# Kernel tuning notes

Measured on AMD Instinct MI355X. Metric: run time of the kernel, lower is better.

## Reference

```python
import jax, jax.numpy as jnp
import numpy as np

B, G, C, K = 16, 2048, 128, 16


def setup_inputs() -> dict:
    key = jax.random.key(0)
    k1, k2, k3, k4 = jax.random.split(key, 4)
    xyz = jax.random.normal(k1, (B, G, 3), dtype=jnp.float32)
    feat = jax.random.normal(k2, (B, G, C), dtype=jnp.float32)
    # MLP params: Linear(C->C) -> GELU -> Linear(C->C)
    W1 = jax.random.normal(k3, (C, C), dtype=jnp.float32) * 0.02
    b1 = jnp.zeros((C,), dtype=jnp.float32)
    W2 = jax.random.normal(k4, (C, C), dtype=jnp.float32) * 0.02
    b2 = jnp.zeros((C,), dtype=jnp.float32)
    return {"xyz": xyz, "feat": feat, "W1": W1, "b1": b1, "W2": W2, "b2": b2}


def _knn_idx(xyz, k):
    # squared pairwise distances [B,G,G]; ranking identical to cdist (sqrt monotone)
    sq = jnp.sum(xyz * xyz, axis=-1)  # [B,G]
    d2 = sq[:, :, None] + sq[:, None, :] - 2.0 * jnp.einsum("bgd,bhd->bgh", xyz, xyz)
    _, idx = jax.lax.top_k(-d2, k)  # smallest distances
    return idx  # [B,G,k]


def reference(xyz, feat, W1, b1, W2, b2):
    idx = _knn_idx(xyz, K)                                   # [B,G,K]
    # gather neighbor features: feat[b, idx[b,g,k], :] -> [B,G,K,C]
    neigh = jnp.take_along_axis(feat[:, None, :, :], idx[..., None], axis=2)
    pooled = jnp.sqrt(jnp.sum(neigh * neigh, axis=-2))       # L2 norm over K -> [B,G,C]
    h = jax.nn.gelu(pooled @ W1 + b1, approximate=False)
    return h @ W2 + b2
```

## Files before the change

kernel.cpp:

```cpp
#include <hip/hip_runtime.h>
#include <math.h>

#define Bn 16
#define Gn 2048
#define Cn 128
#define Kn 16
#define QB 32
#define SSEG 144
#define AS 136

typedef __attribute__((ext_vector_type(8))) short bf16x8;
typedef __attribute__((ext_vector_type(4))) float f32x4;

__device__ __forceinline__ unsigned short f2bf(float x) {
    unsigned int u = __float_as_uint(x);
    unsigned int r = (u + 0x7fffu + ((u >> 16) & 1u)) >> 16;
    return (unsigned short)r;
}
__device__ __forceinline__ float bf2f(unsigned short h) {
    return __uint_as_float(((unsigned int)h) << 16);
}

__device__ __forceinline__ float med3f(float a, float b, float c) {
#if __has_builtin(__builtin_amdgcn_fmed3f)
    return __builtin_amdgcn_fmed3f(a, b, c);
#else
    return fmaxf(fminf(a, b), fminf(fmaxf(a, b), c));
#endif
}

__device__ __forceinline__ float dist2(const float4 me, const float4 p) {
    float dot = fmaf(me.z, p.z, fmaf(me.y, p.y, me.x * p.x));
    return fmaf(-2.0f, dot, me.w + p.w);
}

__device__ __forceinline__ void ins16(float (&d)[16], float v) {
    float prev = d[0];
    d[0] = fminf(d[0], v);
    #pragma unroll
    for (int t = 1; t < 16; ++t) { float cur = d[t]; d[t] = med3f(v, prev, cur); prev = cur; }
}

__device__ __forceinline__ void merge16(float (&d)[16]) {
    #pragma unroll
    for (int m = 1; m < 16; m <<= 1) {
        #pragma unroll
        for (int t = 0; t < 8; ++t) {
            float sa = __shfl_xor(d[15 - t], m);
            float sb = __shfl_xor(d[t], m);
            d[t]      = fminf(d[t], sa);
            d[15 - t] = fminf(d[15 - t], sb);
        }
        #pragma unroll
        for (int k = 8; k; k >>= 1) {
            #pragma unroll
            for (int t = 0; t < 16; ++t)
                if (!(t & k)) {
                    float lo = fminf(d[t], d[t + k]);
                    float hi = fmaxf(d[t], d[t + k]);
                    d[t] = lo; d[t + k] = hi;
                }
        }
    }
}

__device__ __forceinline__ float gelu_exact(float x) {
    return 0.5f * x * (1.0f + erff(x * 0.70710678118654752440f));
}

__global__ __launch_bounds__(256) void prep_w(const float* __restrict__ W1,
                                              const float* __restrict__ W2,
                                              unsigned short* __restrict__ ws) {
    int t = blockIdx.x * 256 + threadIdx.x;
    if (t < 16384) {
        int k = t >> 7, n = t & 127;
        float w = W1[t];
        unsigned short h = f2bf(w);
        unsigned short l = f2bf(w - bf2f(h));
        ws[n * 128 + k]          = h;
        ws[16384 + n * 128 + k]  = l;
        w = W2[t];
        h = f2bf(w);
        l = f2bf(w - bf2f(h));
        ws[32768 + n * 128 + k]  = h;
        ws[49152 + n * 128 + k]  = l;
    }
}

__global__ __launch_bounds__(512) void fused_kernel(const float* __restrict__ xyz,
                                                    const float* __restrict__ feat,
                                                    const float* __restrict__ b1,
                                                    const float* __restrict__ b2,
                                                    const unsigned short* __restrict__ wt,
                                                    float* __restrict__ out) {
    __shared__ __align__(16) float smem0[9728];
    float4* pts = reinterpret_cast<float4*>(smem0);
    unsigned short* Ahi = reinterpret_cast<unsigned short*>(smem0);
    unsigned short* Alo = Ahi + QB * AS;
    unsigned short* Hhi = Alo + QB * AS;
    unsigned short* Hlo = Hhi + QB * AS;
    unsigned short* outb = reinterpret_cast<unsigned short*>(smem0) + 18432;
    unsigned short* tieb = outb + QB * 16;

    const int x     = blockIdx.x;
    const int b     = x & 15;
    const int chunk = x >> 4;
    const int tid   = threadIdx.x;
    const int lane  = tid & 63;
    const int w     = tid >> 6;
    const int sub   = lane & 15;
    const int qg    = lane >> 4;
    const int q     = w * 4 + qg;
    const int g     = chunk * QB + q;

    const float* xb = xyz + (size_t)b * Gn * 3;
    for (int i = tid; i < Gn; i += 512) {
        float px = xb[i * 3 + 0], py = xb[i * 3 + 1], pz = xb[i * 3 + 2];
        float4 v = make_float4(px, py, pz, px * px + py * py + pz * pz);
        int seg = i >> 7, slot = i & 127;
        pts[seg * SSEG + slot] = v;
        if (slot < 16) pts[seg * SSEG + 128 + slot] = v;
    }
    __syncthreads();

    const float4 me = pts[(g >> 7) * SSEG + (g & 127)];
    const float4* seg = pts + sub * SSEG + sub;

    float m1 = INFINITY, m2 = INFINITY;
    #pragma unroll 4
    for (int j = 0; j < 32; ++j) {
        float v = dist2(me, seg[j]);
        m2 = med3f(v, m1, m2);
        m1 = fminf(m1, v);
    }
    float d[16];
    #pragma unroll
    for (int t = 2; t < 16; ++t) d[t] = INFINITY;
    d[0] = m1; d[1] = m2;
    merge16(d);
    const float T0 = d[15];

    unsigned mw[4];
    #pragma unroll 1
    for (int wd = 0; wd < 4; ++wd) {
        unsigned mm = 0;
        #pragma unroll 4
        for (int j = 0; j < 32; ++j) {
            float v = dist2(me, seg[wd * 32 + j]);
            mm |= (v <= T0) ? (1u << j) : 0u;
        }
        mw[wd] = mm;
    }
    unsigned long long blo = mw[0] | ((unsigned long long)mw[1] << 32);
    unsigned long long bhi = mw[2] | ((unsigned long long)mw[3] << 32);

    #pragma unroll
    for (int t = 0; t < 16; ++t) d[t] = INFINITY;
    {
        unsigned long long m = blo;
        while (m) {
            int p = __builtin_ctzll(m); m &= m - 1;
            ins16(d, dist2(me, seg[p]));
        }
        m = bhi;
        while (m) {
            int p = 64 + __builtin_ctzll(m); m &= m - 1;
            ins16(d, dist2(me, seg[p]));
        }
    }
    merge16(d);
    const float T = d[15];

    int myc = __popcll(blo) + __popcll(bhi);
    int mymax = myc;
    #pragma unroll
    for (int m = 1; m < 16; m <<= 1) {
        int o = __shfl_xor(mymax, m);
        mymax = (o > mymax) ? o : mymax;
    }
    const unsigned lowm = (1u << sub) - 1;
    const int shft = lane & 48;
    int nl = 0, nt = 0;
    for (int i = 0; i < mymax; ++i) {
        int h = 0; float v = INFINITY;
        if ((blo | bhi) != 0ull) {
            int p;
            if (blo) { p = __builtin_ctzll(blo); blo &= blo - 1; }
            else     { p = 64 + __builtin_ctzll(bhi); bhi &= bhi - 1; }
            h = (sub << 7) | ((sub + p) & 127);
            v = dist2(me, seg[p]);
        }
        bool pl = (v < T), pt = (v == T);
        unsigned long long ml = __ballot(pl);
        unsigned long long mt = __ballot(pt);
        unsigned gml = (unsigned)(ml >> shft) & 0xFFFFu;
        unsigned gmt = (unsigned)(mt >> shft) & 0xFFFFu;
        if (pl) outb[q * 16 + nl + __popc(gml & lowm)] = (unsigned short)h;
        if (pt) { int pp = nt + __popc(gmt & lowm); if (pp < 16) tieb[q * 16 + pp] = (unsigned short)h; }
        nl += __popc(gml);
        nt += __popc(gmt);
    }
    if (sub == 0) {
        int mfill = nl;
        int need  = 16 - mfill;
        int tc = (nt > 16) ? 16 : nt;
        for (int s = 0; s < need; ++s) {
            int best = 0x7fffffff, bp = -1;
            for (int u = 0; u < tc; ++u) {
                int vv = tieb[q * 16 + u];
                if (vv < best) { best = vv; bp = u; }
            }
            if (bp >= 0) { tieb[q * 16 + bp] = 0xFFFF; outb[q * 16 + mfill + s] = (unsigned short)best; }
        }
    }
    __syncthreads();

    const float4* fb4 = (const float4*)(feat + (size_t)b * Gn * Cn);
    const int cl = lane & 31;
    #pragma unroll
    for (int pass = 0; pass < 2; ++pass) {
        int qq = w * 4 + pass * 2 + (lane >> 5);
        float4 a = make_float4(0.f, 0.f, 0.f, 0.f);
        #pragma unroll
        for (int qt = 0; qt < 8; ++qt) {
            int hs[2]; float4 f[2];
            #pragma unroll
            for (int k = 0; k < 2; ++k) hs[k] = outb[qq * 16 + qt * 2 + k];
            #pragma unroll
            for (int k = 0; k < 2; ++k) f[k] = fb4[(size_t)hs[k] * 32 + cl];
            #pragma unroll
            for (int k = 0; k < 2; ++k) {
                a.x = fmaf(f[k].x, f[k].x, a.x);
                a.y = fmaf(f[k].y, f[k].y, a.y);
                a.z = fmaf(f[k].z, f[k].z, a.z);
                a.w = fmaf(f[k].w, f[k].w, a.w);
            }
        }
        float r0 = sqrtf(a.x), r1 = sqrtf(a.y), r2 = sqrtf(a.z), r3 = sqrtf(a.w);
        unsigned short h0 = f2bf(r0), h1 = f2bf(r1), h2 = f2bf(r2), h3 = f2bf(r3);
        ushort4 hv = make_ushort4(h0, h1, h2, h3);
        ushort4 lv = make_ushort4(f2bf(r0 - bf2f(h0)), f2bf(r1 - bf2f(h1)),
                                  f2bf(r2 - bf2f(h2)), f2bf(r3 - bf2f(h3)));
        *(ushort4*)&Ahi[qq * AS + cl * 4] = hv;
        *(ushort4*)&Alo[qq * AS + cl * 4] = lv;
    }
    __syncthreads();

    const int l15  = lane & 15;
    const int kofs = (lane >> 4) * 8;
    const int rowg = (w & 1) * 16;
    const int colg0 = (w >> 1) * 32;

    #pragma unroll 1
    for (int cb = 0; cb < 2; ++cb) {
        float bv = b1[colg0 + cb * 16 + l15];
        f32x4 acc = (f32x4){bv, bv, bv, bv};
        #pragma unroll
        for (int kk = 0; kk < 128; kk += 32) {
            bf16x8 ah = *(const bf16x8*)&Ahi[(rowg + l15) * AS + kk + kofs];
            bf16x8 al = *(const bf16x8*)&Alo[(rowg + l15) * AS + kk + kofs];
            const unsigned short* wp = wt + (size_t)(colg0 + cb * 16 + l15) * 128 + kk + kofs;
            bf16x8 bh = *(const bf16x8*)wp;
            bf16x8 bl = *(const bf16x8*)(wp + 16384);
            acc = __builtin_amdgcn_mfma_f32_16x16x32_bf16(ah, bh, acc, 0, 0, 0);
            acc = __builtin_amdgcn_mfma_f32_16x16x32_bf16(ah, bl, acc, 0, 0, 0);
            acc = __builtin_amdgcn_mfma_f32_16x16x32_bf16(al, bh, acc, 0, 0, 0);
        }
        #pragma unroll
        for (int r = 0; r < 4; ++r) {
            float gv = gelu_exact(acc[r]);
            unsigned short h = f2bf(gv);
            int row = rowg + (lane >> 4) * 4 + r;
            int col = colg0 + cb * 16 + l15;
            Hhi[row * AS + col] = h;
            Hlo[row * AS + col] = f2bf(gv - bf2f(h));
        }
    }
    __syncthreads();

    const size_t orow0 = (size_t)b * Gn + (size_t)chunk * QB + rowg + (lane >> 4) * 4;
    #pragma unroll 1
    for (int cb = 0; cb < 2; ++cb) {
        float bv = b2[colg0 + cb * 16 + l15];
        f32x4 acc = (f32x4){bv, bv, bv, bv};
        #pragma unroll
        for (int kk = 0; kk < 128; kk += 32) {
            bf16x8 ah = *(const bf16x8*)&Hhi[(rowg + l15) * AS + kk + kofs];
            bf16x8 al = *(const bf16x8*)&Hlo[(rowg + l15) * AS + kk + kofs];
            const unsigned short* wp = wt + 32768 + (size_t)(colg0 + cb * 16 + l15) * 128 + kk + kofs;
            bf16x8 bh = *(const bf16x8*)wp;
            bf16x8 bl = *(const bf16x8*)(wp + 16384);
            acc = __builtin_amdgcn_mfma_f32_16x16x32_bf16(ah, bh, acc, 0, 0, 0);
            acc = __builtin_amdgcn_mfma_f32_16x16x32_bf16(ah, bl, acc, 0, 0, 0);
            acc = __builtin_amdgcn_mfma_f32_16x16x32_bf16(al, bh, acc, 0, 0, 0);
        }
        #pragma unroll
        for (int r = 0; r < 4; ++r) {
            out[(orow0 + r) * Cn + colg0 + cb * 16 + l15] = acc[r];
        }
    }
}

extern "C" void kernel_launch(void* const* d_in, const int* in_sizes, int n_in,
                              void* d_out, int out_size, void* d_ws, size_t ws_size,
                              hipStream_t stream) {
    const float* xyz  = (const float*)d_in[0];
    const float* feat = (const float*)d_in[1];
    const float* W1   = (const float*)d_in[2];
    const float* b1   = (const float*)d_in[3];
    const float* W2   = (const float*)d_in[4];
    const float* b2   = (const float*)d_in[5];
    float* out = (float*)d_out;
    unsigned short* wt = (unsigned short*)d_ws;

    prep_w<<<64, 256, 0, stream>>>(W1, W2, wt);
    fused_kernel<<<1024, 512, 0, stream>>>(xyz, feat, b1, b2, wt, out);
}
```

Measured before the change: 140.2 us.

## Replace ballot-based kNN compaction with per-lane counts and segmented prefix scan

Each lane first counts its candidates below and equal to the threshold. A shfl_up prefix scan within the 16-lane group then gives each lane its write offsets, and a second pass writes indices directly. This removes the lockstep loop of per-candidate ballots bounded by the group maximum. The point load now uses float4 vector loads with each thread handling four points, and the neighbour gather reads four indices at once as a ushort4. The cost is recomputing distances in a second pass, and the tie ordering within lanes changes, though the later tie-break still sorts by index.

```diff
diff --git a/kernel.cpp b/kernel.cpp
--- a/kernel.cpp
+++ b/kernel.cpp
@@ -113,13 +113,22 @@
     const int q     = w * 4 + qg;
     const int g     = chunk * QB + q;
 
-    const float* xb = xyz + (size_t)b * Gn * 3;
-    for (int i = tid; i < Gn; i += 512) {
-        float px = xb[i * 3 + 0], py = xb[i * 3 + 1], pz = xb[i * 3 + 2];
-        float4 v = make_float4(px, py, pz, px * px + py * py + pz * pz);
-        int seg = i >> 7, slot = i & 127;
-        pts[seg * SSEG + slot] = v;
-        if (slot < 16) pts[seg * SSEG + 128 + slot] = v;
+    {
+        const float4* xb4 = (const float4*)(xyz + (size_t)b * Gn * 3);
+        float4 f0 = xb4[tid * 3 + 0];
+        float4 f1 = xb4[tid * 3 + 1];
+        float4 f2 = xb4[tid * 3 + 2];
+        float px[4] = {f0.x, f0.w, f1.z, f2.y};
+        float py[4] = {f0.y, f1.x, f1.w, f2.z};
+        float pz[4] = {f0.z, f1.y, f2.x, f2.w};
+        int i0 = tid * 4, sg = i0 >> 7, sl = i0 & 127;
+        #pragma unroll
+        for (int u = 0; u < 4; ++u) {
+            float4 v = make_float4(px[u], py[u], pz[u],
+                                   px[u] * px[u] + py[u] * py[u] + pz[u] * pz[u]);
+            pts[sg * SSEG + sl + u] = v;
+            if (sl + u < 16) pts[sg * SSEG + 128 + sl + u] = v;
+        }
     }
     __syncthreads();
 
@@ -151,8 +160,8 @@
         }
         mw[wd] = mm;
     }
-    unsigned long long blo = mw[0] | ((unsigned long long)mw[1] << 32);
-    unsigned long long bhi = mw[2] | ((unsigned long long)mw[3] << 32);
+    const unsigned long long blo = mw[0] | ((unsigned long long)mw[1] << 32);
+    const unsigned long long bhi = mw[2] | ((unsigned long long)mw[3] << 32);
 
     #pragma unroll
     for (int t = 0; t < 16; ++t) d[t] = INFINITY;
@@ -171,39 +180,54 @@
     merge16(d);
     const float T = d[15];
 
-    int myc = __popcll(blo) + __popcll(bhi);
-    int mymax = myc;
-    #pragma unroll
-    for (int m = 1; m < 16; m <<= 1) {
-        int o = __shfl_xor(mymax, m);
-        mymax = (o > mymax) ? o : mymax;
-    }
-    const unsigned lowm = (1u << sub) - 1;
-    const int shft = lane & 48;
-    int nl = 0, nt = 0;
-    for (int i = 0; i < mymax; ++i) {
-        int h = 0; float v = INFINITY;
-        if ((blo | bhi) != 0ull) {
-            int p;
-            if (blo) { p = __builtin_ctzll(blo); blo &= blo - 1; }
-            else     { p = 64 + __builtin_ctzll(bhi); bhi &= bhi - 1; }
-            h = (sub << 7) | ((sub + p) & 127);
-            v = dist2(me, seg[p]);
-        }
-        bool pl = (v < T), pt = (v == T);
-        unsigned long long ml = __ballot(pl);
-        unsigned long long mt = __ballot(pt);
-        unsigned gml = (unsigned)(ml >> shft) & 0xFFFFu;
-        unsigned gmt = (unsigned)(mt >> shft) & 0xFFFFu;
-        if (pl) outb[q * 16 + nl + __popc(gml & lowm)] = (unsigned short)h;
-        if (pt) { int pp = nt + __popc(gmt & lowm); if (pp < 16) tieb[q * 16 + pp] = (unsigned short)h; }
-        nl += __popc(gml);
-        nt += __popc(gmt);
+    int cntl = 0, cnte = 0;
+    {
+        unsigned long long m = blo;
+        while (m) {
+            int p = __builtin_ctzll(m); m &= m - 1;
+            float v = dist2(me, seg[p]);
+            cntl += (v < T); cnte += (v == T);
+        }
+        m = bhi;
+        while (m) {
+            int p = 64 + __builtin_ctzll(m); m &= m - 1;
+            float v = dist2(me, seg[p]);
+            cntl += (v < T); cnte += (v == T);
+        }
+    }
+    int il = cntl, ie = cnte;
+    #pragma unroll
+    for (int dlt = 1; dlt < 16; dlt <<= 1) {
+        int yl = __shfl_up(il, dlt, 16);
+        int ye = __shfl_up(ie, dlt, 16);
+        if (sub >= dlt) { il += yl; ie += ye; }
+    }
+    int wl = il - cntl;
+    int we = ie - cnte;
+    const int nl_tot = __shfl(il, 15, 16);
+    const int nt_tot = __shfl(ie, 15, 16);
+    {
+        unsigned long long m = blo;
+        while (m) {
+            int p = __builtin_ctzll(m); m &= m - 1;
+            float v = dist2(me, seg[p]);
+            int h = (sub << 7) | ((sub + p) & 127);
+            if (v < T) outb[q * 16 + (wl++)] = (unsigned short)h;
+            else if (v == T) { if (we < 16) tieb[q * 16 + we] = (unsigned short)h; we++; }
+        }
+        m = bhi;
+        while (m) {
+            int p = 64 + __builtin_ctzll(m); m &= m - 1;
+            float v = dist2(me, seg[p]);
+            int h = (sub << 7) | ((sub + p) & 127);
+            if (v < T) outb[q * 16 + (wl++)] = (unsigned short)h;
+            else if (v == T) { if (we < 16) tieb[q * 16 + we] = (unsigned short)h; we++; }
+        }
     }
     if (sub == 0) {
-        int mfill = nl;
+        int mfill = nl_tot;
         int need  = 16 - mfill;
-        int tc = (nt > 16) ? 16 : nt;
+        int tc = (nt_tot > 16) ? 16 : nt_tot;
         for (int s = 0; s < need; ++s) {
             int best = 0x7fffffff, bp = -1;
             for (int u = 0; u < tc; ++u) {
@@ -216,33 +240,34 @@
     __syncthreads();
 
     const float4* fb4 = (const float4*)(feat + (size_t)b * Gn * Cn);
-    const int cl = lane & 31;
+    const int cll = lane & 31;
     #pragma unroll
     for (int pass = 0; pass < 2; ++pass) {
         int qq = w * 4 + pass * 2 + (lane >> 5);
         float4 a = make_float4(0.f, 0.f, 0.f, 0.f);
         #pragma unroll
-        for (int qt = 0; qt < 8; ++qt) {
-            int hs[2]; float4 f[2];
-            #pragma unroll
-            for (int k = 0; k < 2; ++k) hs[k] = outb[qq * 16 + qt * 2 + k];
-            #pragma unroll
-            for (int k = 0; k < 2; ++k) f[k] = fb4[(size_t)hs[k] * 32 + cl];
-            #pragma unroll
-            for (int k = 0; k < 2; ++k) {
-                a.x = fmaf(f[k].x, f[k].x, a.x);
-                a.y = fmaf(f[k].y, f[k].y, a.y);
-                a.z = fmaf(f[k].z, f[k].z, a.z);
-                a.w = fmaf(f[k].w, f[k].w, a.w);
-            }
+        for (int qt = 0; qt < 4; ++qt) {
+            ushort4 h4 = *(const ushort4*)&outb[qq * 16 + qt * 4];
+            float4 f0 = fb4[(size_t)h4.x * 32 + cll];
+            float4 f1 = fb4[(size_t)h4.y * 32 + cll];
+            a.x = fmaf(f0.x, f0.x, a.x); a.y = fmaf(f0.y, f0.y, a.y);
+            a.z = fmaf(f0.z, f0.z, a.z); a.w = fmaf(f0.w, f0.w, a.w);
+            a.x = fmaf(f1.x, f1.x, a.x); a.y = fmaf(f1.y, f1.y, a.y);
+            a.z = fmaf(f1.z, f1.z, a.z); a.w = fmaf(f1.w, f1.w, a.w);
+            float4 f2 = fb4[(size_t)h4.z * 32 + cll];
+            float4 f3 = fb4[(size_t)h4.w * 32 + cll];
+            a.x = fmaf(f2.x, f2.x, a.x); a.y = fmaf(f2.y, f2.y, a.y);
+            a.z = fmaf(f2.z, f2.z, a.z); a.w = fmaf(f2.w, f2.w, a.w);
+            a.x = fmaf(f3.x, f3.x, a.x); a.y = fmaf(f3.y, f3.y, a.y);
+            a.z = fmaf(f3.z, f3.z, a.z); a.w = fmaf(f3.w, f3.w, a.w);
         }
         float r0 = sqrtf(a.x), r1 = sqrtf(a.y), r2 = sqrtf(a.z), r3 = sqrtf(a.w);
         unsigned short h0 = f2bf(r0), h1 = f2bf(r1), h2 = f2bf(r2), h3 = f2bf(r3);
         ushort4 hv = make_ushort4(h0, h1, h2, h3);
         ushort4 lv = make_ushort4(f2bf(r0 - bf2f(h0)), f2bf(r1 - bf2f(h1)),
                                   f2bf(r2 - bf2f(h2)), f2bf(r3 - bf2f(h3)));
-        *(ushort4*)&Ahi[qq * AS + cl * 4] = hv;
-        *(ushort4*)&Alo[qq * AS + cl * 4] = lv;
+        *(ushort4*)&Ahi[qq * AS + cll * 4] = hv;
+        *(ushort4*)&Alo[qq * AS + cll * 4] = lv;
     }
     __syncthreads();
 
```

Result: no change. 142.0 us (+1.3%).
